# Optimization experiments

Measured on AMD Instinct MI355X. Metric: run time of the kernel, lower is better.

## Reference

```python
import jax, jax.numpy as jnp
import numpy as np

K = 4          # neighbors
R = 2          # step_ratio
OUT = 64       # output_size

def knn_idx(x, k):
    # x: (B, C, N) -> indices of k nearest neighbors (incl. self): (B, N, k)
    xx = jnp.sum(x * x, axis=1)                       # (B, N)
    inner = jnp.einsum('bcn,bcm->bnm', x, x)          # (B, N, N)
    neg_dist = 2.0 * inner - xx[:, :, None] - xx[:, None, :]
    _, idx = jax.lax.top_k(neg_dist, k)               # largest neg_dist = nearest
    return idx

def setup_inputs() -> dict:
    key = jax.random.key(0)
    ks = jax.random.split(key, 7)
    B, C, N = 16, 64, 2048
    s = 0.05
    return {
        'x':  jax.random.normal(ks[0], (B, C, N), jnp.float32),
        'w1': jax.random.normal(ks[1], (OUT, 2 * C), jnp.float32) * s,
        'b1': jax.random.normal(ks[2], (OUT,), jnp.float32) * s,
        'w2': jax.random.normal(ks[3], (OUT * R, 2 * C + OUT), jnp.float32) * s,
        'b2': jax.random.normal(ks[4], (OUT * R,), jnp.float32) * s,
        'w3': jax.random.normal(ks[5], (OUT, OUT), jnp.float32) * s,
        'b3': jax.random.normal(ks[6], (OUT,), jnp.float32) * s,
    }

def reference(x, w1, b1, w2, b2, w3, b3):
    B, C, N = x.shape
    idx = knn_idx(x, K)                                # (B, N, K)
    xt = jnp.transpose(x, (0, 2, 1))                   # (B, N, C)
    neighbors = xt[jnp.arange(B)[:, None, None], idx]  # (B, N, K, C)
    center = jnp.broadcast_to(xt[:, :, None, :], neighbors.shape)
    feat = jnp.concatenate([center, neighbors], axis=-1)   # (B, N, K, 2C), minus_center=False
    # get_graph_feature returns (B, 2C, N, K); module permutes to (B, 2C, K, N)
    f = jnp.transpose(feat, (0, 3, 2, 1))              # (B, 2C, K, N)
    e1 = jnp.einsum('oc,bckn->bokn', w1, f) + b1[None, :, None, None]
    e = jax.nn.relu(jnp.concatenate([e1, f], axis=1))  # (B, 2C+OUT, K, N)
    e2 = jax.nn.relu(jnp.einsum('oc,bckn->bokn', w2, e) + b2[None, :, None, None])  # (B, OUT*R, K, N)
    # permute(0,2,3,1) -> (B,K,N,OUT*R), view -> (B,K,N*R,OUT), permute -> (B,OUT,K,N*R)
    e2 = jnp.transpose(e2, (0, 2, 3, 1)).reshape(B, K, N * R, OUT)
    e2 = jnp.transpose(e2, (0, 3, 1, 2))               # (B, OUT, K, N*R)
    e3 = jnp.einsum('oc,bckn->bokn', w3, e2) + b3[None, :, None, None]
    return jnp.max(e3, axis=2)                          # (B, OUT, N*R)
```

## Files before the change

kernel.cpp:

```cpp
#include <hip/hip_runtime.h>
#include <hip/hip_bf16.h>

#define BB 16
#define CC 64
#define NN 2048
#define KK 4
#define NPART 4
#define JPER (NN / NPART)
#define NCAND 32
#define RSTRIDE 80

typedef unsigned short u16;
typedef unsigned int u32;
typedef __attribute__((ext_vector_type(4))) float f32x4;
typedef __attribute__((ext_vector_type(16))) float f32x16;
typedef __attribute__((ext_vector_type(8))) short short8;

__device__ __forceinline__ float bf2f(u16 u) {
    unsigned int x = ((unsigned int)u) << 16;
    float f;
    __builtin_memcpy(&f, &x, 4);
    return f;
}
__device__ __forceinline__ u16 f2bf(float f) {
    __hip_bfloat16 h = __float2bfloat16(f);
    u16 u;
    __builtin_memcpy(&u, &h, 2);
    return u;
}
__device__ __forceinline__ unsigned int pk2(float a, float b) {
    return (unsigned int)f2bf(a) | ((unsigned int)f2bf(b) << 16);
}
__device__ __forceinline__ u32 umx(u32 a, u32 b) { return a > b ? a : b; }
__device__ __forceinline__ u32 umn(u32 a, u32 b) { return a < b ? a : b; }

__global__ __launch_bounds__(256) void k_prep(const float* __restrict__ x,
                                              float* __restrict__ xt,
                                              u16* __restrict__ xpk) {
    int b = blockIdx.y;
    int n = blockIdx.x * 256 + threadIdx.x;
    const float* xb = x + (size_t)b * CC * NN;
    float v[CC];
    float s = 0.f;
#pragma unroll
    for (int c = 0; c < CC; c++) {
        v[c] = xb[(size_t)c * NN + n];
        s = fmaf(v[c], v[c], s);
    }
    float4* dst = (float4*)(xt + ((size_t)b * NN + n) * CC);
#pragma unroll
    for (int q = 0; q < 16; q++) {
        dst[q] = make_float4(v[4 * q], v[4 * q + 1], v[4 * q + 2], v[4 * q + 3]);
    }
    u16* dp = xpk + ((size_t)b * NN + n) * RSTRIDE;
#pragma unroll
    for (int q = 0; q < 8; q++) {
        uint4 u;
        u.x = pk2(v[8 * q], v[8 * q + 1]);
        u.y = pk2(v[8 * q + 2], v[8 * q + 3]);
        u.z = pk2(v[8 * q + 4], v[8 * q + 5]);
        u.w = pk2(v[8 * q + 6], v[8 * q + 7]);
        *(uint4*)(dp + q * 8) = u;
    }
    u16 hi = f2bf(s);
    u16 lo = f2bf(s - bf2f(hi));
    uint4 u8;
    u8.x = (unsigned int)hi | ((unsigned int)lo << 16);
    u8.y = 0x00003F80u;
    u8.z = 0; u8.w = 0;
    *(uint4*)(dp + 64) = u8;
    uint4 z = {0, 0, 0, 0};
    *(uint4*)(dp + 72) = z;
}

__global__ __launch_bounds__(256) void k_wprep(const float* __restrict__ w1,
                                               const float* __restrict__ w2,
                                               const float* __restrict__ w3,
                                               u16* __restrict__ wb1,
                                               u16* __restrict__ wb2,
                                               u16* __restrict__ wb3) {
    int t = blockIdx.x * 256 + threadIdx.x;
    int stride = gridDim.x * 256;
    for (int idx = t; idx < 64 * 128; idx += stride) {
        int o = idx >> 7, k = idx & 127;
        int cb = o >> 4, lr = o & 15, ks = k >> 5, g = (k >> 3) & 3, e = k & 7;
        wb1[((cb * 4 + ks) * 64 + g * 16 + lr) * 8 + e] = f2bf(w1[idx]);
    }
    for (int idx = t; idx < 128 * 192; idx += stride) {
        int o = idx / 192, k = idx - o * 192;
        int cb = o >> 4, lr = o & 15, ks = k >> 5, g = (k >> 3) & 3, e = k & 7;
        wb2[((cb * 6 + ks) * 64 + g * 16 + lr) * 8 + e] = f2bf(w2[idx]);
    }
    for (int idx = t; idx < 64 * 64; idx += stride) {
        int o = idx >> 6, k = idx & 63;
        int cb = o >> 4, lr = o & 15, ks = k >> 5, g = (k >> 3) & 3, e = k & 7;
        wb3[((cb * 2 + ks) * 64 + g * 16 + lr) * 8 + e] = f2bf(w3[idx]);
    }
}

__global__ __launch_bounds__(256) void k_knn3(const u16* __restrict__ xpk,
                                              u16* __restrict__ cand) {
    int ib = blockIdx.x;
    int part = blockIdx.y;
    int b = blockIdx.z;
    int tid = threadIdx.x;
    int i0 = ib * 128;
    int j00 = part * JPER;

    __shared__ u16 Bb[2 * 2 * 10 * 32 * 8];

    int w = tid >> 6, l = tid & 63;
    int lc = l & 31, lh = l >> 5;
    int hb4 = lh * 4;

    short8 ifrag[5];
    {
        const u16* ip = xpk + ((size_t)b * NN + i0 + w * 32 + lc) * RSTRIDE + lh * 8;
#pragma unroll
        for (int ks = 0; ks < 4; ks++) ifrag[ks] = *(const short8*)(ip + ks * 16);
        short8 f4 = {0, 0, 0, 0, 0, 0, 0, 0};
        if (lh == 0) {
            f4[0] = (short)0xBF00;
            f4[1] = (short)0xBF00;
            f4[2] = (short)0x4300;
        }
        ifrag[4] = f4;
    }

    u32 v0 = 0, v1 = 0, v2 = 0, v3 = 0;

#define CE(a, b) { u32 mx_ = umx(a, b); b = umn(a, b); a = mx_; }

#define STAGE(rr, bf)                                                              \
    {                                                                              \
        int jb = j00 + (rr) * 64;                                                  \
        for (int g = tid; g < 640; g += 256) {                                     \
            int rw = g / 10, c = g - rw * 10;                                      \
            uint4 u = *(const uint4*)(xpk + ((size_t)b * NN + jb + rw) * RSTRIDE + \
                                      c * 8);                                      \
            int sub = rw >> 5, r32 = rw & 31;                                      \
            *(uint4*)((char*)Bb + (bf) * 10240 + sub * 5120 + c * 512 +            \
                      ((r32 ^ (c & 7)) * 16)) = u;                                 \
        }                                                                          \
    }

    STAGE(0, 0);

    for (int r = 0; r < JPER / 64; r++) {
        __syncthreads();
        if (r + 1 < JPER / 64) STAGE(r + 1, (r + 1) & 1);

        const char* bufp = (const char*)Bb + (r & 1) * 10240;
        f32x16 acc0, acc1;
#pragma unroll
        for (int e = 0; e < 16; e++) {
            acc0[e] = 0.f;
            acc1[e] = 0.f;
        }
#pragma unroll
        for (int ks = 0; ks < 5; ks++) {
            int c = ks * 2 + lh;
            int boff = c * 512 + ((lc ^ (c & 7)) * 16);
            short8 a0 = *(const short8*)(bufp + boff);
            short8 a1 = *(const short8*)(bufp + 5120 + boff);
            acc0 = __builtin_amdgcn_mfma_f32_32x32x16_bf16(a0, ifrag[ks], acc0, 0, 0, 0);
            acc1 = __builtin_amdgcn_mfma_f32_32x32x16_bf16(a1, ifrag[ks], acc1, 0, 0, 0);
        }
#pragma unroll
        for (int sub = 0; sub < 2; sub++) {
            const f32x16& acc = sub ? acc1 : acc0;
            int jlb = r * 64 + sub * 32 + hb4;
            u32 kk[16];
#pragma unroll
            for (int rg = 0; rg < 16; rg++) {
                u32 u;
                float f = acc[rg];
                __builtin_memcpy(&u, &f, 4);
                int coff = (rg & 3) + 8 * (rg >> 2);
                kk[rg] = (u & ~0x1FFu) | (u32)(jlb + coff);
            }
#pragma unroll
            for (int q = 0; q < 4; q++) {
                int p = q * 4;
                CE(kk[p + 0], kk[p + 2]); CE(kk[p + 1], kk[p + 3]);
                CE(kk[p + 0], kk[p + 1]); CE(kk[p + 2], kk[p + 3]);
                CE(kk[p + 1], kk[p + 2]);
            }
            kk[0] = umx(kk[0], kk[7]); kk[1] = umx(kk[1], kk[6]);
            kk[2] = umx(kk[2], kk[5]); kk[3] = umx(kk[3], kk[4]);
            CE(kk[0], kk[2]); CE(kk[1], kk[3]); CE(kk[0], kk[1]); CE(kk[2], kk[3]);
            kk[8] = umx(kk[8], kk[15]); kk[9] = umx(kk[9], kk[14]);
            kk[10] = umx(kk[10], kk[13]); kk[11] = umx(kk[11], kk[12]);
            CE(kk[8], kk[10]); CE(kk[9], kk[11]); CE(kk[8], kk[9]); CE(kk[10], kk[11]);
            kk[0] = umx(kk[0], kk[11]); kk[1] = umx(kk[1], kk[10]);
            kk[2] = umx(kk[2], kk[9]); kk[3] = umx(kk[3], kk[8]);
            CE(kk[0], kk[2]); CE(kk[1], kk[3]); CE(kk[0], kk[1]); CE(kk[2], kk[3]);
            v0 = umx(v0, kk[3]); v1 = umx(v1, kk[2]);
            v2 = umx(v2, kk[1]); v3 = umx(v3, kk[0]);
            CE(v0, v2); CE(v1, v3); CE(v0, v1); CE(v2, v3);
        }
    }
#undef STAGE
#undef CE

    size_t cb = ((size_t)b * NN + i0 + w * 32 + lc) * NCAND + part * 8 + lh * 4;
    cand[cb + 0] = (u16)(j00 + (v0 & 0x1FF));
    cand[cb + 1] = (u16)(j00 + (v1 & 0x1FF));
    cand[cb + 2] = (u16)(j00 + (v2 & 0x1FF));
    cand[cb + 3] = (u16)(j00 + (v3 & 0x1FF));
}

__global__ __launch_bounds__(256) void k_knn_merge(const float* __restrict__ xt,
                                                   const u16* __restrict__ cand,
                                                   int* __restrict__ nidx) {
    __shared__ double sv[32 * 33];
    __shared__ int si[32 * 33];

    int tid = threadIdx.x;
    int pl = tid >> 3;
    int sub = tid & 7;
    int gp = blockIdx.x * 32 + pl;
    int b = gp >> 11;
    int i = gp & (NN - 1);

    const float* xrow = xt + ((size_t)b * NN + i) * CC;
    float xi[CC];
#pragma unroll
    for (int q = 0; q < 16; q++) {
        float4 t = ((const float4*)xrow)[q];
        xi[4 * q] = t.x; xi[4 * q + 1] = t.y; xi[4 * q + 2] = t.z; xi[4 * q + 3] = t.w;
    }
    double xxi = 0.0;
#pragma unroll
    for (int c = 0; c < CC; c++) xxi += (double)xi[c] * (double)xi[c];

    size_t base = (size_t)gp * NCAND + sub * 4;
#pragma unroll
    for (int cc = 0; cc < 4; cc++) {
        int j = cand[base + cc];
        const float* xj = xt + ((size_t)b * NN + j) * CC;
        double dot = 0.0, sj = 0.0;
#pragma unroll
        for (int q = 0; q < 16; q++) {
            float4 t = ((const float4*)xj)[q];
            double b0 = (double)t.x, b1 = (double)t.y, b2v = (double)t.z, b3v = (double)t.w;
            dot += (double)xi[4 * q] * b0 + (double)xi[4 * q + 1] * b1 +
                   (double)xi[4 * q + 2] * b2v + (double)xi[4 * q + 3] * b3v;
            sj += b0 * b0 + b1 * b1 + b2v * b2v + b3v * b3v;
        }
        int c = sub * 4 + cc;
        sv[c * 33 + pl] = 2.0 * dot - xxi - sj;
        si[c * 33 + pl] = j;
    }
    __syncthreads();

    if (tid < 32) {
        int p = tid;
        double v4[4];
        int id4[4];
#pragma unroll
        for (int s = 0; s < 4; s++) {
            v4[s] = -1e300;
            id4[s] = 0x7fffffff;
        }
        for (int c = 0; c < NCAND; c++) {
            double cv = sv[c * 33 + p];
            int ci = si[c * 33 + p];
#pragma unroll
            for (int s = 0; s < 4; s++) {
                bool take = (cv > v4[s]) || (cv == v4[s] && ci < id4[s]);
                double nv = take ? cv : v4[s];
                int ni = take ? ci : id4[s];
                double ov = take ? v4[s] : cv;
                int oi = take ? id4[s] : ci;
                v4[s] = nv;
                id4[s] = ni;
                cv = ov;
                ci = oi;
            }
        }
        size_t gp2 = (size_t)blockIdx.x * 32 + p;
#pragma unroll
        for (int s = 0; s < 4; s++) nidx[gp2 * 4 + s] = id4[s];
    }
}

__global__ __launch_bounds__(256) void k_mlp(const u16* __restrict__ xpk,
                                             const int* __restrict__ nidx,
                                             const u16* __restrict__ wb1,
                                             const u16* __restrict__ wb2,
                                             const u16* __restrict__ wb3,
                                             const float* __restrict__ b1,
                                             const float* __restrict__ b2,
                                             const float* __restrict__ b3,
                                             float* __restrict__ out) {
    int nch = blockIdx.x;
    int b = blockIdx.y;
    int n0 = nch * 16;
    int tid = threadIdx.x;

    __shared__ u16 Fb[64 * 128];
    __shared__ u16 E1b[64 * 64];
    __shared__ u16 E2b[64 * 128];
    __shared__ float Ob[64 * 36];
    __shared__ int ji[64];

    if (tid < 64) ji[tid] = nidx[((size_t)b * NN + n0) * KK + tid];
    __syncthreads();

    for (int g = tid; g < 64 * 16; g += 256) {
        int it = g >> 4, q = g & 15;
        int half = q >> 3, cq = q & 7;
        int srcn = half ? ji[it] : (n0 + (it >> 2));
        uint4 u = *(const uint4*)(xpk + ((size_t)b * NN + srcn) * RSTRIDE + cq * 8);
        int byte = (it * 256 + half * 128 + cq * 16) ^ ((it & 7) << 4);
        *(uint4*)((char*)Fb + byte) = u;
    }
    __syncthreads();

    int w = tid >> 6, l = tid & 63;
    int lr = l & 15, lg = l >> 4;

    {
        f32x4 acc[4];
#pragma unroll
        for (int g = 0; g < 4; g++) acc[g] = (f32x4){0.f, 0.f, 0.f, 0.f};
#pragma unroll
        for (int ks = 0; ks < 4; ks++) {
            short8 bw = *(const short8*)(wb1 + ((size_t)(w * 4 + ks) * 64 + l) * 8);
#pragma unroll
            for (int g = 0; g < 4; g++) {
                int arow = g * 16 + lr;
                int off = (arow * 256 + ks * 64 + lg * 16) ^ ((arow & 7) << 4);
                short8 a = *(const short8*)((const char*)Fb + off);
                acc[g] = __builtin_amdgcn_mfma_f32_16x16x32_bf16(a, bw, acc[g], 0, 0, 0);
            }
        }
        float bias = b1[w * 16 + lr];
#pragma unroll
        for (int g = 0; g < 4; g++) {
#pragma unroll
            for (int q = 0; q < 4; q++) {
                int item = g * 16 + lg * 4 + q;
                float vv = fmaxf(acc[g][q] + bias, 0.f);
                int byte = (item * 128 + (w * 16 + lr) * 2) ^ ((item & 7) << 4);
                *(u16*)((char*)E1b + byte) = f2bf(vv);
            }
        }
    }
    __syncthreads();

    {
        f32x4 acc[4][2];
#pragma unroll
        for (int g = 0; g < 4; g++)
#pragma unroll
            for (int c2 = 0; c2 < 2; c2++) acc[g][c2] = (f32x4){0.f, 0.f, 0.f, 0.f};
#pragma unroll
        for (int ks = 0; ks < 6; ks++) {
            short8 bw0 = *(const short8*)(wb2 + ((size_t)((w * 2) * 6 + ks) * 64 + l) * 8);
            short8 bw1 = *(const short8*)(wb2 + ((size_t)((w * 2 + 1) * 6 + ks) * 64 + l) * 8);
#pragma unroll
            for (int g = 0; g < 4; g++) {
                int arow = g * 16 + lr;
                int aswz = (arow & 7) << 4;
                short8 a;
                if (ks < 2) {
                    int off = (arow * 128 + ks * 64 + lg * 16) ^ aswz;
                    a = *(const short8*)((const char*)E1b + off);
                } else {
                    int off = (arow * 256 + (ks - 2) * 64 + lg * 16) ^ aswz;
                    uint4 u = *(const uint4*)((const char*)Fb + off);
                    unsigned int m;
                    m = ((u.x >> 15) & 0x10001u) * 0xFFFFu; u.x &= ~m;
                    m = ((u.y >> 15) & 0x10001u) * 0xFFFFu; u.y &= ~m;
                    m = ((u.z >> 15) & 0x10001u) * 0xFFFFu; u.z &= ~m;
                    m = ((u.w >> 15) & 0x10001u) * 0xFFFFu; u.w &= ~m;
                    __builtin_memcpy(&a, &u, 16);
                }
                acc[g][0] = __builtin_amdgcn_mfma_f32_16x16x32_bf16(a, bw0, acc[g][0], 0, 0, 0);
                acc[g][1] = __builtin_amdgcn_mfma_f32_16x16x32_bf16(a, bw1, acc[g][1], 0, 0, 0);
            }
        }
#pragma unroll
        for (int c2 = 0; c2 < 2; c2++) {
            float bias = b2[(w * 2 + c2) * 16 + lr];
#pragma unroll
            for (int g = 0; g < 4; g++) {
#pragma unroll
                for (int q = 0; q < 4; q++) {
                    int item = g * 16 + lg * 4 + q;
                    float vv = fmaxf(acc[g][c2][q] + bias, 0.f);
                    int byte = (item * 256 + ((w * 2 + c2) * 16 + lr) * 2) ^ ((item & 7) << 4);
                    *(u16*)((char*)E2b + byte) = f2bf(vv);
                }
            }
        }
    }
    __syncthreads();

    {
        f32x4 acc[4][2];
#pragma unroll
        for (int g = 0; g < 4; g++)
#pragma unroll
            for (int r = 0; r < 2; r++) acc[g][r] = (f32x4){0.f, 0.f, 0.f, 0.f};
#pragma unroll
        for (int ks = 0; ks < 2; ks++) {
            short8 bw = *(const short8*)(wb3 + ((size_t)(w * 2 + ks) * 64 + l) * 8);
#pragma unroll
            for (int g = 0; g < 4; g++) {
                int arow = g * 16 + lr;
                int aswz = (arow & 7) << 4;
#pragma unroll
                for (int r = 0; r < 2; r++) {
                    int off = (arow * 256 + r * 128 + ks * 64 + lg * 16) ^ aswz;
                    short8 a = *(const short8*)((const char*)E2b + off);
                    acc[g][r] = __builtin_amdgcn_mfma_f32_16x16x32_bf16(a, bw, acc[g][r], 0, 0, 0);
                }
            }
        }
        float bias = b3[w * 16 + lr];
        int o = w * 16 + lr;
#pragma unroll
        for (int g = 0; g < 4; g++) {
            int nl = g * 4 + lg;
#pragma unroll
            for (int r = 0; r < 2; r++) {
                float m = fmaxf(fmaxf(acc[g][r][0], acc[g][r][1]),
                                fmaxf(acc[g][r][2], acc[g][r][3])) + bias;
                Ob[o * 36 + nl * 2 + r] = m;
            }
        }
    }
    __syncthreads();

    {
        int o = tid >> 2, q = tid & 3;
        float4 v0 = *(const float4*)&Ob[o * 36 + q * 8];
        float4 v1 = *(const float4*)&Ob[o * 36 + q * 8 + 4];
        float* dst = out + ((size_t)(b * 64 + o)) * 4096 + n0 * 2 + q * 8;
        ((float4*)dst)[0] = v0;
        ((float4*)dst)[1] = v1;
    }
}

extern "C" void kernel_launch(void* const* d_in, const int* in_sizes, int n_in,
                              void* d_out, int out_size, void* d_ws, size_t ws_size,
                              hipStream_t stream) {
    const float* x = (const float*)d_in[0];
    const float* w1 = (const float*)d_in[1];
    const float* b1 = (const float*)d_in[2];
    const float* w2 = (const float*)d_in[3];
    const float* b2 = (const float*)d_in[4];
    const float* w3 = (const float*)d_in[5];
    const float* b3 = (const float*)d_in[6];
    float* out = (float*)d_out;

    float* xt = (float*)d_ws;
    u16* xpk = (u16*)(xt + (size_t)BB * NN * CC);
    int* nidx = (int*)(xpk + (size_t)BB * NN * RSTRIDE);
    u16* cand = (u16*)(nidx + (size_t)BB * NN * KK);
    u16* wb1 = cand + (size_t)BB * NN * NCAND;
    u16* wb2 = wb1 + 64 * 128;
    u16* wb3 = wb2 + 128 * 192;

    k_prep<<<dim3(NN / 256, BB), 256, 0, stream>>>(x, xt, xpk);
    k_wprep<<<dim3(32), 256, 0, stream>>>(w1, w2, w3, wb1, wb2, wb3);
    k_knn3<<<dim3(NN / 128, NPART, BB), 256, 0, stream>>>(xpk, cand);
    k_knn_merge<<<dim3(BB * NN / 32), 256, 0, stream>>>(xt, cand, nidx);
    k_mlp<<<dim3(NN / 16, BB), 256, 0, stream>>>(xpk, nidx, wb1, wb2, wb3, b1, b2, b3, out);
}
```

Before: 118.5 us.

## Rework KNN merge to one thread per candidate and drop constant self-norm

The candidate rescoring kernel now handles 8 points per block with one thread per candidate (32 threads per point), instead of 32 points per block with 8 threads each computing 4 candidates. Each thread streams the center and candidate rows directly rather than caching the center row in 64 registers. The xxi term is dropped because it is constant per point and does not change the top-k order. This aims to cut register pressure and serial FP64 work per thread, at the cost of 4x more blocks, redundant center-row loads, and fewer lanes active in the serial top-4 merge.

```diff
diff --git a/kernel.cpp b/kernel.cpp
--- a/kernel.cpp
+++ b/kernel.cpp
@@ -213,48 +213,38 @@
 __global__ __launch_bounds__(256) void k_knn_merge(const float* __restrict__ xt,
                                                    const u16* __restrict__ cand,
                                                    int* __restrict__ nidx) {
-    __shared__ double sv[32 * 33];
-    __shared__ int si[32 * 33];
+    __shared__ double sv[8 * 33];
+    __shared__ int si[8 * 33];
 
     int tid = threadIdx.x;
-    int pl = tid >> 3;
-    int sub = tid & 7;
-    int gp = blockIdx.x * 32 + pl;
-    int b = gp >> 11;
-    int i = gp & (NN - 1);
-
-    const float* xrow = xt + ((size_t)b * NN + i) * CC;
-    float xi[CC];
-#pragma unroll
-    for (int q = 0; q < 16; q++) {
-        float4 t = ((const float4*)xrow)[q];
-        xi[4 * q] = t.x; xi[4 * q + 1] = t.y; xi[4 * q + 2] = t.z; xi[4 * q + 3] = t.w;
-    }
-    double xxi = 0.0;
-#pragma unroll
-    for (int c = 0; c < CC; c++) xxi += (double)xi[c] * (double)xi[c];
-
-    size_t base = (size_t)gp * NCAND + sub * 4;
-#pragma unroll
-    for (int cc = 0; cc < 4; cc++) {
-        int j = cand[base + cc];
-        const float* xj = xt + ((size_t)b * NN + j) * CC;
-        double dot = 0.0, sj = 0.0;
-#pragma unroll
-        for (int q = 0; q < 16; q++) {
-            float4 t = ((const float4*)xj)[q];
-            double b0 = (double)t.x, b1 = (double)t.y, b2v = (double)t.z, b3v = (double)t.w;
-            dot += (double)xi[4 * q] * b0 + (double)xi[4 * q + 1] * b1 +
-                   (double)xi[4 * q + 2] * b2v + (double)xi[4 * q + 3] * b3v;
-            sj += b0 * b0 + b1 * b1 + b2v * b2v + b3v * b3v;
-        }
-        int c = sub * 4 + cc;
-        sv[c * 33 + pl] = 2.0 * dot - xxi - sj;
-        si[c * 33 + pl] = j;
-    }
-    __syncthreads();
-
-    if (tid < 32) {
+    int pl = tid >> 5;
+    int c = tid & 31;
+    size_t gp = (size_t)blockIdx.x * 8 + pl;
+    int b = (int)(gp >> 11);
+
+    int j = cand[gp * NCAND + c];
+    const float4* xi = (const float4*)(xt + gp * CC);
+    const float4* xj = (const float4*)(xt + (((size_t)b << 11) + j) * CC);
+
+    double d0 = 0.0, d1 = 0.0, s0 = 0.0, s1 = 0.0;
+#pragma unroll
+    for (int q = 0; q < 16; q += 2) {
+        float4 a0 = xi[q], a1 = xi[q + 1];
+        float4 c0 = xj[q], c1 = xj[q + 1];
+        d0 += (double)a0.x * c0.x + (double)a0.y * c0.y +
+              (double)a0.z * c0.z + (double)a0.w * c0.w;
+        s0 += (double)c0.x * c0.x + (double)c0.y * c0.y +
+              (double)c0.z * c0.z + (double)c0.w * c0.w;
+        d1 += (double)a1.x * c1.x + (double)a1.y * c1.y +
+              (double)a1.z * c1.z + (double)a1.w * c1.w;
+        s1 += (double)c1.x * c1.x + (double)c1.y * c1.y +
+              (double)c1.z * c1.z + (double)c1.w * c1.w;
+    }
+    sv[pl * 33 + c] = 2.0 * (d0 + d1) - (s0 + s1);
+    si[pl * 33 + c] = j;
+    __syncthreads();
+
+    if (tid < 8) {
         int p = tid;
         double v4[4];
         int id4[4];
@@ -263,9 +253,9 @@
             v4[s] = -1e300;
             id4[s] = 0x7fffffff;
         }
-        for (int c = 0; c < NCAND; c++) {
-            double cv = sv[c * 33 + p];
-            int ci = si[c * 33 + p];
+        for (int cc = 0; cc < NCAND; cc++) {
+            double cv = sv[p * 33 + cc];
+            int ci = si[p * 33 + cc];
 #pragma unroll
             for (int s = 0; s < 4; s++) {
                 bool take = (cv > v4[s]) || (cv == v4[s] && ci < id4[s]);
@@ -279,7 +269,7 @@
                 ci = oi;
             }
         }
-        size_t gp2 = (size_t)blockIdx.x * 32 + p;
+        size_t gp2 = (size_t)blockIdx.x * 8 + p;
 #pragma unroll
         for (int s = 0; s < 4; s++) nidx[gp2 * 4 + s] = id4[s];
     }
@@ -468,6 +458,6 @@
     k_prep<<<dim3(NN / 256, BB), 256, 0, stream>>>(x, xt, xpk);
     k_wprep<<<dim3(32), 256, 0, stream>>>(w1, w2, w3, wb1, wb2, wb3);
     k_knn3<<<dim3(NN / 128, NPART, BB), 256, 0, stream>>>(xpk, cand);
-    k_knn_merge<<<dim3(BB * NN / 32), 256, 0, stream>>>(xt, cand, nidx);
+    k_knn_merge<<<dim3(BB * NN / 8), 256, 0, stream>>>(xt, cand, nidx);
     k_mlp<<<dim3(NN / 16, BB), 256, 0, stream>>>(xpk, nidx, wb1, wb2, wb3, b1, b2, b3, out);
 }
```

New measurement: 119.5 us. About the same (+0.8%).
